# Performance work log

Hardware: AMD Instinct MI355X
Metric: run time of the kernel (lower is better)

## Reference

```python
import jax, jax.numpy as jnp
import numpy as np
import math

F_DIM = 512
N_HEADS = 8
HEAD_DIM = F_DIM // N_HEADS
IMG = 16            # image_size
L = IMG ** 3        # voxel sequence length = 4096
PATCH = 196         # patch_number (ViT 14x14)
VIT_RES = 14
RES = 224           # VIEW_IMAGE_RES
SKETCH_DIM = 768
SIGMA = 1.5         # fixed kernel_size (torch draws randomly when None)
GN_GROUPS = 32


def position_encoding(d_model, length):
    pe = np.zeros((length, d_model), dtype=np.float32)
    position = np.arange(length, dtype=np.float32)[:, None]
    div_term = np.exp(np.arange(0, d_model, 2, dtype=np.float32) * -(math.log(10000.0) / d_model))
    pe[:, 0::2] = np.sin(position * div_term)
    pe[:, 1::2] = np.cos(position * div_term)
    return jnp.asarray(pe)


def get_voxel_coordinates(resolution, size=1.0):
    # centers of a resolution^3 grid spanning [-size/2, size/2]
    idx = np.arange(resolution, dtype=np.float32)
    g = np.stack(np.meshgrid(idx, idx, idx, indexing='ij'), -1).reshape(-1, 3)
    return (g + 0.5) / resolution * size - size / 2.0


VOXEL_PE = position_encoding(F_DIM, L)          # (L, F)
COND_PE = position_encoding(F_DIM, PATCH)       # (S, F)
VOXEL_PTS = jnp.asarray(get_voxel_coordinates(IMG))  # (L, 3)
_vg = np.arange(VIT_RES, dtype=np.float32)
VIT_PIXELS = jnp.asarray(np.stack(np.meshgrid(_vg, _vg, indexing='ij'), -1).reshape(PATCH, 2))  # (S, 2)


def setup_inputs() -> dict:
    key = jax.random.key(0)
    ks = jax.random.split(key, 12)
    B = 8
    s = 0.02
    return {
        'x': jax.random.normal(ks[0], (B, F_DIM, IMG, IMG, IMG), jnp.float32),
        'sketch_feature': jax.random.normal(ks[1], (B, PATCH, SKETCH_DIM), jnp.float32),
        'projection_matrix': jax.random.normal(ks[2], (B, 1, 3, 3), jnp.float32),
        'gn_scale': jnp.ones((F_DIM,), jnp.float32),
        'gn_bias': jnp.zeros((F_DIM,), jnp.float32),
        'conv_w': jax.random.normal(ks[3], (F_DIM, F_DIM, 3, 3, 3), jnp.float32) * s,
        'conv_b': jnp.zeros((F_DIM,), jnp.float32),
        'k_w': jax.random.normal(ks[4], (F_DIM, SKETCH_DIM), jnp.float32) * s,
        'k_b': jnp.zeros((F_DIM,), jnp.float32),
        'v_w': jax.random.normal(ks[5], (F_DIM, SKETCH_DIM), jnp.float32) * s,
        'v_b': jnp.zeros((F_DIM,), jnp.float32),
        'in_proj_w': jax.random.normal(ks[6], (3 * F_DIM, F_DIM), jnp.float32) * s,
        'in_proj_b': jnp.zeros((3 * F_DIM,), jnp.float32),
        'out_w': jax.random.normal(ks[7], (F_DIM, F_DIM), jnp.float32) * s,
        'out_b': jnp.zeros((F_DIM,), jnp.float32),
    }


def _group_norm(x, scale, bias, groups=GN_GROUPS, eps=1e-5):
    B, C = x.shape[0], x.shape[1]
    xr = x.reshape(B, groups, C // groups, -1)
    m = xr.mean(axis=(2, 3), keepdims=True)
    v = xr.var(axis=(2, 3), keepdims=True)
    xn = ((xr - m) / jnp.sqrt(v + eps)).reshape(x.shape)
    shp = (1, C) + (1,) * (x.ndim - 2)
    return xn * scale.reshape(shp) + bias.reshape(shp)


def _attn_mask(projection_matrix):
    # project voxel centers, clamp to pixel grid, threshold cdist to vit patch centers
    P = projection_matrix[:, 0]                                  # (B,3,3)
    pc = jnp.einsum('bij,nj->bni', P, VOXEL_PTS)                 # (B,L,3)
    pixels = pc[..., 0:2] / pc[..., 2:3]
    pixels = jnp.clip(jnp.round(pixels), 0.0, RES - 1.0)         # clamp_pixel
    x_idx = (2.0 * pixels[..., 1:2] + 1.0) / RES * VIT_RES / 2.0
    y_idx = (2.0 * (RES - 1.0 - pixels[..., 0:1]) + 1.0) / RES * VIT_RES / 2.0
    ps = jnp.concatenate([x_idx, y_idx], -1) - 0.5               # (B,L,2)
    dist = jnp.linalg.norm(ps[:, :, None, :] - VIT_PIXELS[None, None], axis=-1)  # (B,L,S)
    return jnp.abs(dist) > (SIGMA - 1e-6)                        # True = masked out


def _forward(x, sketch_feature, projection_matrix, gn_scale, gn_bias, conv_w, conv_b,
             k_w, k_b, v_w, v_b, in_proj_w, in_proj_b, out_w, out_b):
    B = x.shape[0]
    # q path: GroupNorm -> SiLU -> Conv3d(3, pad 1)
    h = jax.nn.silu(_group_norm(x, gn_scale, gn_bias))
    h = jax.lax.conv_general_dilated(h, conv_w, window_strides=(1, 1, 1),
                                     padding=[(1, 1)] * 3,
                                     dimension_numbers=('NCDHW', 'OIDHW', 'NCDHW'))
    h = h + conv_b.reshape(1, F_DIM, 1, 1, 1)
    q = h.reshape(B, F_DIM, L).transpose(0, 2, 1) + VOXEL_PE[None]        # (B,L,F)

    mask = _attn_mask(projection_matrix)                                   # (B,L,S)

    k = sketch_feature @ k_w.T + k_b + COND_PE[None]                       # (B,S,F)
    v = sketch_feature @ v_w.T + v_b + COND_PE[None]

    # nn.MultiheadAttention (eval: no dropout)
    wq, wk, wv = jnp.split(in_proj_w, 3, axis=0)
    bq, bk, bv = jnp.split(in_proj_b, 3, axis=0)
    qh = (q @ wq.T + bq).reshape(B, L, N_HEADS, HEAD_DIM).transpose(0, 2, 1, 3)
    kh = (k @ wk.T + bk).reshape(B, PATCH, N_HEADS, HEAD_DIM).transpose(0, 2, 1, 3)
    vh = (v @ wv.T + bv).reshape(B, PATCH, N_HEADS, HEAD_DIM).transpose(0, 2, 1, 3)

    scores = jnp.einsum('bhld,bhsd->bhls', qh, kh) / math.sqrt(HEAD_DIM)   # (B,H,L,S)
    scores = jnp.where(mask[:, None], -jnp.inf, scores)                    # mask shared over heads
    attn = jax.nn.softmax(scores, axis=-1)
    o = jnp.einsum('bhls,bhsd->bhld', attn, vh)
    o = o.transpose(0, 2, 1, 3).reshape(B, L, F_DIM)
    o = o @ out_w.T + out_b                                                # (B,L,F)
    return o.transpose(0, 2, 1).reshape(B, F_DIM, IMG, IMG, IMG)


def reference(x, sketch_feature, projection_matrix, gn_scale, gn_bias, conv_w, conv_b,
              k_w, k_b, v_w, v_b, in_proj_w, in_proj_b, out_w, out_b):
    return _forward(x, sketch_feature, projection_matrix, gn_scale, gn_bias, conv_w, conv_b,
                    k_w, k_b, v_w, v_b, in_proj_w, in_proj_b, out_w, out_b)
```

## Files before the change

### kernel.cpp

```cpp
#include <hip/hip_runtime.h>

#define DEV static __device__ __forceinline__

typedef unsigned short u16;
typedef unsigned int u32;
typedef unsigned long long u64;
typedef float f32x4 __attribute__((ext_vector_type(4)));
typedef short bfrag __attribute__((ext_vector_type(8)));

#define FD 512
#define LV 4096
#define PV 5832

DEV float b2f(u16 u){ union{ u32 i; float f; } x; x.i = ((u32)u)<<16; return x.f; }
DEV u16 f2b(float f){ union{ float f; u32 i; } x; x.f = f; u32 r = x.i; r += 0x7fffu + ((r>>16)&1u); return (u16)(r>>16); }

DEV void g2l(const void* g, void* s){
  __builtin_amdgcn_global_load_lds((const __attribute__((address_space(1))) void*)g,
                                   (__attribute__((address_space(3))) void*)s, 16, 0, 0);
}

static const size_t o_wt  = 0;
static const size_t o_wq  = 14155776;
static const size_t o_ow  = 14680064;
static const size_t o_vpe = 15204352;
static const size_t o_cpe = 23592960;
static const size_t o_gn  = 23994368;
static const size_t o_mask= 23996416;
static const size_t o_khb = 25044992;
static const size_t o_vhb = 26748928;
static const size_t o_hp  = 36841472;
static const size_t o_qb  = 84617216;
static const size_t o_qh  = 118171648;
static const size_t o_skb = o_qh;
static const size_t o_kwb = o_qh + 2555904;
static const size_t o_vwb = o_qh + 3342336;
static const size_t o_wkb = o_qh + 4128768;
static const size_t o_wvb = o_qh + 4653056;
static const size_t o_ktb = o_qh + 5177344;
static const size_t o_vtb = o_qh + 6881280;

__global__ void pe_kernel(float* __restrict__ pe, int length){
  int l = blockIdx.x;
  int i = threadIdx.x;
  if (l >= length) return;
  const float fac = -0.017988946039015984f;
  float dt = expf((float)(2*i) * fac);
  float ang = (float)l * dt;
  pe[(size_t)l*FD + 2*i]     = sinf(ang);
  pe[(size_t)l*FD + 2*i + 1] = cosf(ang);
}

__global__ void cast_bf16(const float* __restrict__ in, u16* __restrict__ out, int n){
  int i = blockIdx.x*256 + threadIdx.x;
  if (i < n) out[i] = f2b(in[i]);
}

__global__ void convw_prep(const float* __restrict__ cw, u16* __restrict__ wt){
  int idx = blockIdx.x*256 + threadIdx.x;
  const float* src = cw + (size_t)idx*27;
  float v[27];
  #pragma unroll
  for (int k=0;k<27;k++) v[k] = src[k];
  #pragma unroll
  for (int k=0;k<27;k++) wt[(size_t)k*262144 + idx] = f2b(v[k]);
}

__global__ __launch_bounds__(256) void gn_stats(const float* __restrict__ x, float* __restrict__ stats){
  int bg = blockIdx.x;
  const float* base = x + (size_t)bg*65536;
  float s=0.f, q=0.f;
  for (int i=threadIdx.x;i<65536;i+=256){ float v = base[i]; s+=v; q+=v*v; }
  #pragma unroll
  for (int off=32; off>0; off>>=1){ s += __shfl_xor(s,off); q += __shfl_xor(q,off); }
  __shared__ float red[8];
  int w = threadIdx.x>>6;
  if ((threadIdx.x&63)==0){ red[w*2]=s; red[w*2+1]=q; }
  __syncthreads();
  if (threadIdx.x==0){
    float S=red[0]+red[2]+red[4]+red[6];
    float Q=red[1]+red[3]+red[5]+red[7];
    float m = S*(1.f/65536.f);
    float var = Q*(1.f/65536.f) - m*m;
    stats[bg] = m;
    stats[256+bg] = rsqrtf(var + 1e-5f);
  }
}

__global__ __launch_bounds__(256) void gn_apply_b(const float* __restrict__ x,
    const float* __restrict__ stats, const float* __restrict__ sc, const float* __restrict__ bi,
    u16* __restrict__ hp){
  int zb = blockIdx.x, cb = blockIdx.y, b = blockIdx.z;
  const float* xb = x + (size_t)b*FD*LV;
  u16* hpb = hp + (size_t)b*PV*FD;
  int t = threadIdx.x;
  int y = t>>4, xx = t&15;
  size_t hrow = ((size_t)(zb+1)*324 + (size_t)(y+1)*18 + (xx+1))*FD;
  int v = zb*256 + t;
  #pragma unroll 4
  for (int cc=0; cc<64; ++cc){
    int c = cb*64 + cc;
    float val = xb[(size_t)c*LV + v];
    int g = c>>4;
    float m = stats[b*32+g];
    float r = stats[256 + b*32+g];
    float xn = (val - m)*r*sc[c] + bi[c];
    hpb[hrow + c] = f2b(xn / (1.f + expf(-xn)));
  }
}

__global__ __launch_bounds__(256,4) void conv_mfma(const u16* __restrict__ hp,
    const u16* __restrict__ wt, const float* __restrict__ cbias,
    const float* __restrict__ vpe, u16* __restrict__ qb){
  __shared__ __align__(16) u16 Al[8192];
  __shared__ __align__(16) u16 Wl[8192];
  int tid = threadIdx.x;
  int w = tid>>6, l = tid&63;
  int v0 = blockIdx.x*128, n0 = blockIdx.y*128, b = blockIdx.z;
  int swz = ((l&7) ^ ((l>>3)&7))*8;
  size_t abase[4], wbase[4];
  #pragma unroll
  for (int j=0;j<4;j++){
    int r = w*32 + j*8 + (l>>3);
    int v = v0 + r;
    int z = v>>8, yy=(v>>4)&15, xx=v&15;
    abase[j] = ((size_t)b*PV + (size_t)(z*324 + yy*18 + xx))*FD + swz;
    wbase[j] = (size_t)(n0 + r)*FD + swz;
  }
  f32x4 zero4 = {0.f,0.f,0.f,0.f};
  f32x4 acc[4][4];
  #pragma unroll
  for (int i=0;i<4;i++)
    #pragma unroll
    for (int j=0;j<4;j++) acc[i][j] = zero4;
  int wr = (w>>1)*64, wc = (w&1)*64;
  for (int kk=0; kk<216; ++kk){
    int off = kk>>3;
    int ks  = (kk&7)<<6;
    int dz = off/9; int rem = off - dz*9; int dy = rem/3; int dx = rem - dy*3;
    size_t adelta = (size_t)(dz*324 + dy*18 + dx)*FD + ks;
    size_t wdelta = (size_t)off*262144 + ks;
    #pragma unroll
    for (int j=0;j<4;j++){
      g2l(hp + abase[j] + adelta, Al + (w*32 + j*8)*64);
      g2l(wt + wbase[j] + wdelta, Wl + (w*32 + j*8)*64);
    }
    __syncthreads();
    #pragma unroll
    for (int ks2=0; ks2<2; ++ks2){
      bfrag af[4], wf[4];
      #pragma unroll
      for (int i=0;i<4;i++){
        int ra = wr + i*16 + (l&15);
        af[i] = *(const bfrag*)(Al + ra*64 + (((ks2<<2) + (l>>4)) ^ (l&7))*8);
        int rb = wc + i*16 + (l&15);
        wf[i] = *(const bfrag*)(Wl + rb*64 + (((ks2<<2) + (l>>4)) ^ (l&7))*8);
      }
      #pragma unroll
      for (int i=0;i<4;i++)
        #pragma unroll
        for (int j=0;j<4;j++)
          acc[i][j] = __builtin_amdgcn_mfma_f32_16x16x32_bf16(af[i], wf[j], acc[i][j], 0,0,0);
    }
    __syncthreads();
  }
  #pragma unroll
  for (int i=0;i<4;i++)
    #pragma unroll
    for (int j=0;j<4;j++)
      #pragma unroll
      for (int rg=0;rg<4;rg++){
        int row = wr + i*16 + ((l>>4)<<2) + rg;
        int col = wc + j*16 + (l&15);
        int v = v0 + row, n = n0 + col;
        float cv = acc[i][j][rg] + cbias[n] + vpe[(size_t)v*FD + n];
        qb[((size_t)b*LV + v)*FD + n] = f2b(cv);
      }
}

template<bool TRANS>
__global__ __launch_bounds__(256,2) void gemm_mfma(const u16* __restrict__ A, const u16* __restrict__ W,
    const float* __restrict__ bias, void* __restrict__ Cout){
  __shared__ __align__(16) u16 Al[4096];
  __shared__ __align__(16) u16 Wl[4096];
  int tid = threadIdx.x;
  int w = tid>>6, l = tid&63;
  int m0 = blockIdx.x*128, n0 = blockIdx.y*128, b = blockIdx.z;
  int sw_src = (((l&3) ^ ((l>>3)&3)))*8;
  int sw_rd  = (((l>>4) ^ ((l>>1)&3)))*8;
  size_t abase[2], wbase[2];
  #pragma unroll
  for (int j=0;j<2;j++){
    int r = (w*2+j)*16 + (l>>2);
    abase[j] = ((size_t)b*LV + m0 + r)*FD + sw_src;
    wbase[j] = (size_t)(n0 + r)*FD + sw_src;
  }
  f32x4 zero4 = {0.f,0.f,0.f,0.f};
  f32x4 acc[4][4];
  #pragma unroll
  for (int i=0;i<4;i++)
    #pragma unroll
    for (int j=0;j<4;j++) acc[i][j] = zero4;
  int wr = (w>>1)*64, wc = (w&1)*64;
  for (int k0=0; k0<512; k0+=32){
    #pragma unroll
    for (int j=0;j<2;j++){
      g2l(A + abase[j] + k0, Al + (w*2+j)*512);
      g2l(W + wbase[j] + k0, Wl + (w*2+j)*512);
    }
    __syncthreads();
    bfrag af[4], wf[4];
    #pragma unroll
    for (int i=0;i<4;i++){
      int r  = wr + i*16 + (l&15);
      af[i] = *(const bfrag*)(Al + r*32 + sw_rd);
      int cn = wc + i*16 + (l&15);
      wf[i] = *(const bfrag*)(Wl + cn*32 + sw_rd);
    }
    #pragma unroll
    for (int i=0;i<4;i++)
      #pragma unroll
      for (int j=0;j<4;j++)
        acc[i][j] = __builtin_amdgcn_mfma_f32_16x16x32_bf16(af[i], wf[j], acc[i][j], 0,0,0);
    __syncthreads();
  }
  #pragma unroll
  for (int i=0;i<4;i++)
    #pragma unroll
    for (int j=0;j<4;j++)
      #pragma unroll
      for (int rg=0;rg<4;rg++){
        int row = m0 + wr + i*16 + ((l>>4)<<2) + rg;
        int col = n0 + wc + j*16 + (l&15);
        float cv = acc[i][j][rg] + bias[col];
        if constexpr (TRANS)
          ((float*)Cout)[((size_t)b*FD + col)*LV + row] = cv;
        else
          ((u16*)Cout)[((size_t)b*LV + row)*FD + col] = f2b(cv);
      }
}

template<bool OUTF32, bool ADDPE>
__global__ __launch_bounds__(256,2) void gemm_kv(const u16* __restrict__ A, const u16* __restrict__ W,
    const float* __restrict__ bias, const float* __restrict__ pe,
    void* __restrict__ Cout, int K){
  __shared__ __align__(16) u16 Al[4096];
  __shared__ __align__(16) u16 Wl[4096];
  int tid = threadIdx.x;
  int w = tid>>6, l = tid&63;
  int m0 = blockIdx.x*128, n0 = blockIdx.y*128;
  int sw_src = (((l&3) ^ ((l>>3)&3)))*8;
  int sw_rd  = (((l>>4) ^ ((l>>1)&3)))*8;
  size_t abase[2], wbase[2];
  #pragma unroll
  for (int j=0;j<2;j++){
    int r = (w*2+j)*16 + (l>>2);
    abase[j] = (size_t)(m0 + r)*K + sw_src;
    wbase[j] = (size_t)(n0 + r)*K + sw_src;
  }
  f32x4 zero4 = {0.f,0.f,0.f,0.f};
  f32x4 acc[4][4];
  #pragma unroll
  for (int i=0;i<4;i++)
    #pragma unroll
    for (int j=0;j<4;j++) acc[i][j] = zero4;
  int wr = (w>>1)*64, wc = (w&1)*64;
  for (int k0=0; k0<K; k0+=32){
    #pragma unroll
    for (int j=0;j<2;j++){
      g2l(A + abase[j] + k0, Al + (w*2+j)*512);
      g2l(W + wbase[j] + k0, Wl + (w*2+j)*512);
    }
    __syncthreads();
    bfrag af[4], wf[4];
    #pragma unroll
    for (int i=0;i<4;i++){
      int r  = wr + i*16 + (l&15);
      af[i] = *(const bfrag*)(Al + r*32 + sw_rd);
      int cn = wc + i*16 + (l&15);
      wf[i] = *(const bfrag*)(Wl + cn*32 + sw_rd);
    }
    #pragma unroll
    for (int i=0;i<4;i++)
      #pragma unroll
      for (int j=0;j<4;j++)
        acc[i][j] = __builtin_amdgcn_mfma_f32_16x16x32_bf16(af[i], wf[j], acc[i][j], 0,0,0);
    __syncthreads();
  }
  #pragma unroll
  for (int i=0;i<4;i++)
    #pragma unroll
    for (int j=0;j<4;j++)
      #pragma unroll
      for (int rg=0;rg<4;rg++){
        int row = m0 + wr + i*16 + ((l>>4)<<2) + rg;
        int col = n0 + wc + j*16 + (l&15);
        float cv = acc[i][j][rg] + bias[col];
        if constexpr (ADDPE) cv += pe[(size_t)(row % 196)*FD + col];
        if constexpr (OUTF32) ((float*)Cout)[(size_t)row*FD + col] = cv;
        else                  ((u16*)Cout)[(size_t)row*FD + col] = f2b(cv);
      }
}

__global__ __launch_bounds__(256) void mask_kernel(const float* __restrict__ proj, u64* __restrict__ maskb){
  int idx = blockIdx.x*256 + threadIdx.x;
  int b = idx >> 12, v = idx & 4095;
  float P[9];
  #pragma unroll
  for (int j=0;j<9;j++) P[j] = proj[b*9 + j];
  int zi=v>>8, yi=(v>>4)&15, xi=v&15;
  float pt0 = ((float)zi + 0.5f)/16.0f - 0.5f;
  float pt1 = ((float)yi + 0.5f)/16.0f - 0.5f;
  float pt2 = ((float)xi + 0.5f)/16.0f - 0.5f;
  float pc0 = __fadd_rn(__fadd_rn(__fmul_rn(P[0],pt0), __fmul_rn(P[1],pt1)), __fmul_rn(P[2],pt2));
  float pc1 = __fadd_rn(__fadd_rn(__fmul_rn(P[3],pt0), __fmul_rn(P[4],pt1)), __fmul_rn(P[5],pt2));
  float pc2 = __fadd_rn(__fadd_rn(__fmul_rn(P[6],pt0), __fmul_rn(P[7],pt1)), __fmul_rn(P[8],pt2));
  float r0 = __fdiv_rn(pc0, pc2);
  float r1 = __fdiv_rn(pc1, pc2);
  float px0 = fminf(fmaxf(rintf(r0), 0.f), 223.f);
  float px1 = fminf(fmaxf(rintf(r1), 0.f), 223.f);
  float x_idx = __fmul_rn(__fdiv_rn(__fadd_rn(__fmul_rn(2.f,px1),1.f), 224.f), 14.f) * 0.5f;
  float y_idx = __fmul_rn(__fdiv_rn(__fadd_rn(__fmul_rn(2.f,__fadd_rn(223.f,-px0)),1.f), 224.f), 14.f) * 0.5f;
  float ps0 = __fadd_rn(x_idx, -0.5f);
  float ps1 = __fadd_rn(y_idx, -0.5f);
  const float TH = 1.4999990463256836f;
  u64 abits[4] = {0,0,0,0};
  #pragma unroll 1
  for (int s=0;s<196;s++){
    int si = s/14, sj = s - si*14;
    float d0 = __fadd_rn(ps0, -(float)si);
    float d1 = __fadd_rn(ps1, -(float)sj);
    float dist = sqrtf(__fadd_rn(__fmul_rn(d0,d0), __fmul_rn(d1,d1)));
    if (!(fabsf(dist) > TH)) abits[s>>6] |= (1ull << (s&63));
  }
  u64* out = maskb + (size_t)idx*4;
  out[0]=abits[0]; out[1]=abits[1]; out[2]=abits[2]; out[3]=abits[3];
}

__global__ __launch_bounds__(256) void attn_lit(const u16* __restrict__ qh,
    const u16* __restrict__ khb, const u16* __restrict__ vhb,
    const u64* __restrict__ maskb, u16* __restrict__ obuf){
  int v = blockIdx.x*256 + threadIdx.x;
  int h = blockIdx.y, b = blockIdx.z;
  const u64* mrow = maskb + ((size_t)b*LV + v)*4;
  u64 abits[4] = {mrow[0], mrow[1], mrow[2], mrow[3]};

  float qr[64];
  {
    const uint4* qp = (const uint4*)(qh + ((size_t)b*LV + v)*FD + h*64);
    #pragma unroll
    for (int c=0;c<8;c++){
      uint4 u = qp[c];
      qr[c*8+0]=b2f((u16)(u.x&0xffffu)); qr[c*8+1]=b2f((u16)(u.x>>16));
      qr[c*8+2]=b2f((u16)(u.y&0xffffu)); qr[c*8+3]=b2f((u16)(u.y>>16));
      qr[c*8+4]=b2f((u16)(u.z&0xffffu)); qr[c*8+5]=b2f((u16)(u.z>>16));
      qr[c*8+6]=b2f((u16)(u.w&0xffffu)); qr[c*8+7]=b2f((u16)(u.w>>16));
    }
  }
  const u16* kb = khb + (size_t)(b*196)*FD + h*64;
  const u16* vb = vhb + (size_t)(b*196)*FD + h*64;
  float o[64];
  #pragma unroll
  for (int d=0;d<64;d++) o[d]=0.f;
  float ssum = 0.f;
  for (int s=0;s<196;s++){
    if (!((abits[s>>6] >> (s&63)) & 1ull)) continue;
    const uint4* kr = (const uint4*)(kb + (size_t)s*FD);
    float dot = 0.f;
    #pragma unroll
    for (int c=0;c<8;c++){
      uint4 u = kr[c];
      dot += qr[c*8+0]*b2f((u16)(u.x&0xffffu)) + qr[c*8+1]*b2f((u16)(u.x>>16))
           + qr[c*8+2]*b2f((u16)(u.y&0xffffu)) + qr[c*8+3]*b2f((u16)(u.y>>16))
           + qr[c*8+4]*b2f((u16)(u.z&0xffffu)) + qr[c*8+5]*b2f((u16)(u.z>>16))
           + qr[c*8+6]*b2f((u16)(u.w&0xffffu)) + qr[c*8+7]*b2f((u16)(u.w>>16));
    }
    float e = expf(dot*0.125f);
    ssum += e;
    const uint4* vr = (const uint4*)(vb + (size_t)s*FD);
    #pragma unroll
    for (int c=0;c<8;c++){
      uint4 u = vr[c];
      o[c*8+0] += e*b2f((u16)(u.x&0xffffu)); o[c*8+1] += e*b2f((u16)(u.x>>16));
      o[c*8+2] += e*b2f((u16)(u.y&0xffffu)); o[c*8+3] += e*b2f((u16)(u.y>>16));
      o[c*8+4] += e*b2f((u16)(u.z&0xffffu)); o[c*8+5] += e*b2f((u16)(u.z>>16));
      o[c*8+6] += e*b2f((u16)(u.w&0xffffu)); o[c*8+7] += e*b2f((u16)(u.w>>16));
    }
  }
  float inv = (ssum > 0.f) ? 1.f/ssum : 0.f;
  u32* op = (u32*)(obuf + ((size_t)b*LV + v)*FD + h*64);
  #pragma unroll
  for (int c=0;c<32;c++){
    u32 lo = f2b(o[c*2]*inv);
    u32 hi = f2b(o[c*2+1]*inv);
    op[c] = lo | (hi<<16);
  }
}

extern "C" void kernel_launch(void* const* d_in, const int* in_sizes, int n_in,
                              void* d_out, int out_size, void* d_ws, size_t ws_size,
                              hipStream_t stream) {
  (void)in_sizes; (void)n_in; (void)out_size; (void)ws_size;
  const float* x_in  = (const float*)d_in[0];
  const float* sketch= (const float*)d_in[1];
  const float* projm = (const float*)d_in[2];
  const float* gnsc  = (const float*)d_in[3];
  const float* gnbi  = (const float*)d_in[4];
  const float* convw = (const float*)d_in[5];
  const float* convb = (const float*)d_in[6];
  const float* kw_in = (const float*)d_in[7];
  const float* kb_in = (const float*)d_in[8];
  const float* vw_in = (const float*)d_in[9];
  const float* vb_in = (const float*)d_in[10];
  const float* ipw   = (const float*)d_in[11];
  const float* ipb   = (const float*)d_in[12];
  const float* ow_in = (const float*)d_in[13];
  const float* ob_in = (const float*)d_in[14];
  char* ws = (char*)d_ws;
  u16*   wt   = (u16*)(ws + o_wt);
  u16*   Wq   = (u16*)(ws + o_wq);
  u16*   Ow   = (u16*)(ws + o_ow);
  float* vpe  = (float*)(ws + o_vpe);
  float* cpe  = (float*)(ws + o_cpe);
  float* stats= (float*)(ws + o_gn);
  u64*   maskb= (u64*)(ws + o_mask);
  u16*   khb  = (u16*)(ws + o_khb);
  u16*   vhb  = (u16*)(ws + o_vhb);
  u16*   hp   = (u16*)(ws + o_hp);
  u16*   qb   = (u16*)(ws + o_qb);
  u16*   qhb  = (u16*)(ws + o_qh);
  u16*   Skb  = (u16*)(ws + o_skb);
  u16*   Kwb  = (u16*)(ws + o_kwb);
  u16*   Vwb  = (u16*)(ws + o_vwb);
  u16*   Wkb  = (u16*)(ws + o_wkb);
  u16*   Wvb  = (u16*)(ws + o_wvb);
  u16*   ktb  = (u16*)(ws + o_ktb);
  u16*   vtb  = (u16*)(ws + o_vtb);
  u16*   obuf = qb;

  hipMemsetAsync(hp, 0, 47775744, stream);
  hipMemsetAsync((char*)Skb + 2408448, 0, 147456, stream);
  convw_prep<<<1024,256,0,stream>>>(convw, wt);
  cast_bf16<<<1024,256,0,stream>>>(ipw,          Wq,  262144);
  cast_bf16<<<1024,256,0,stream>>>(ow_in,        Ow,  262144);
  cast_bf16<<<4704,256,0,stream>>>(sketch,       Skb, 1204224);
  cast_bf16<<<1536,256,0,stream>>>(kw_in,        Kwb, 393216);
  cast_bf16<<<1536,256,0,stream>>>(vw_in,        Vwb, 393216);
  cast_bf16<<<1024,256,0,stream>>>(ipw + 262144, Wkb, 262144);
  cast_bf16<<<1024,256,0,stream>>>(ipw + 524288, Wvb, 262144);
  pe_kernel<<<4096,256,0,stream>>>(vpe, 4096);
  pe_kernel<<<196,256,0,stream>>>(cpe, 196);
  gn_stats<<<256,256,0,stream>>>(x_in, stats);
  mask_kernel<<<128,256,0,stream>>>(projm, maskb);
  gemm_kv<false,true ><<<dim3(13,4),256,0,stream>>>(Skb, Kwb, kb_in,      cpe,     ktb, 768);
  gemm_kv<false,true ><<<dim3(13,4),256,0,stream>>>(Skb, Vwb, vb_in,      cpe,     vtb, 768);
  gemm_kv<false,false><<<dim3(13,4),256,0,stream>>>(ktb, Wkb, ipb + 512,  nullptr, khb, 512);
  gemm_kv<false,false><<<dim3(13,4),256,0,stream>>>(vtb, Wvb, ipb + 1024, nullptr, vhb, 512);

  gn_apply_b<<<dim3(16,8,8),256,0,stream>>>(x_in, stats, gnsc, gnbi, hp);
  conv_mfma<<<dim3(32,4,8),256,0,stream>>>(hp, wt, convb, vpe, qb);
  gemm_mfma<false><<<dim3(32,4,8),256,0,stream>>>(qb, Wq, ipb, qhb);
  attn_lit<<<dim3(16,8,8),256,0,stream>>>(qhb, khb, vhb, maskb, obuf);
  gemm_mfma<true ><<<dim3(32,4,8),256,0,stream>>>(obuf, Ow, ob_in, d_out);
}
```

Baseline: 804.2 us.

## Merge prep kernels and batch K/V GEMMs to cut launch count

Folds the eight cast kernels and the conv-weight transpose into one prep_all launch, merges the positional-encoding and mask kernels into geom_prep, and runs the K and V projection GEMMs as one launch each using blockIdx.z to pick the operand set. This removes many small launches and their serialization gaps, and lets the tiny K/V GEMMs fill more CUs. The transposed output GEMM now writes float4 vectors instead of scalar stores. The merged kernels use block-range dispatch, which adds some branching and hardcoded block boundaries.

```diff
diff --git a/kernel.cpp b/kernel.cpp
--- a/kernel.cpp
+++ b/kernel.cpp
@@ -40,270 +40,43 @@
 static const size_t o_ktb = o_qh + 5177344;
 static const size_t o_vtb = o_qh + 6881280;
 
-__global__ void pe_kernel(float* __restrict__ pe, int length){
-  int l = blockIdx.x;
-  int i = threadIdx.x;
-  if (l >= length) return;
-  const float fac = -0.017988946039015984f;
-  float dt = expf((float)(2*i) * fac);
-  float ang = (float)l * dt;
-  pe[(size_t)l*FD + 2*i]     = sinf(ang);
-  pe[(size_t)l*FD + 2*i + 1] = cosf(ang);
-}
-
-__global__ void cast_bf16(const float* __restrict__ in, u16* __restrict__ out, int n){
-  int i = blockIdx.x*256 + threadIdx.x;
-  if (i < n) out[i] = f2b(in[i]);
-}
-
-__global__ void convw_prep(const float* __restrict__ cw, u16* __restrict__ wt){
-  int idx = blockIdx.x*256 + threadIdx.x;
-  const float* src = cw + (size_t)idx*27;
-  float v[27];
-  #pragma unroll
-  for (int k=0;k<27;k++) v[k] = src[k];
-  #pragma unroll
-  for (int k=0;k<27;k++) wt[(size_t)k*262144 + idx] = f2b(v[k]);
-}
-
-__global__ __launch_bounds__(256) void gn_stats(const float* __restrict__ x, float* __restrict__ stats){
-  int bg = blockIdx.x;
-  const float* base = x + (size_t)bg*65536;
-  float s=0.f, q=0.f;
-  for (int i=threadIdx.x;i<65536;i+=256){ float v = base[i]; s+=v; q+=v*v; }
-  #pragma unroll
-  for (int off=32; off>0; off>>=1){ s += __shfl_xor(s,off); q += __shfl_xor(q,off); }
-  __shared__ float red[8];
-  int w = threadIdx.x>>6;
-  if ((threadIdx.x&63)==0){ red[w*2]=s; red[w*2+1]=q; }
-  __syncthreads();
-  if (threadIdx.x==0){
-    float S=red[0]+red[2]+red[4]+red[6];
-    float Q=red[1]+red[3]+red[5]+red[7];
-    float m = S*(1.f/65536.f);
-    float var = Q*(1.f/65536.f) - m*m;
-    stats[bg] = m;
-    stats[256+bg] = rsqrtf(var + 1e-5f);
-  }
-}
-
-__global__ __launch_bounds__(256) void gn_apply_b(const float* __restrict__ x,
-    const float* __restrict__ stats, const float* __restrict__ sc, const float* __restrict__ bi,
-    u16* __restrict__ hp){
-  int zb = blockIdx.x, cb = blockIdx.y, b = blockIdx.z;
-  const float* xb = x + (size_t)b*FD*LV;
-  u16* hpb = hp + (size_t)b*PV*FD;
-  int t = threadIdx.x;
-  int y = t>>4, xx = t&15;
-  size_t hrow = ((size_t)(zb+1)*324 + (size_t)(y+1)*18 + (xx+1))*FD;
-  int v = zb*256 + t;
-  #pragma unroll 4
-  for (int cc=0; cc<64; ++cc){
-    int c = cb*64 + cc;
-    float val = xb[(size_t)c*LV + v];
-    int g = c>>4;
-    float m = stats[b*32+g];
-    float r = stats[256 + b*32+g];
-    float xn = (val - m)*r*sc[c] + bi[c];
-    hpb[hrow + c] = f2b(xn / (1.f + expf(-xn)));
-  }
-}
-
-__global__ __launch_bounds__(256,4) void conv_mfma(const u16* __restrict__ hp,
-    const u16* __restrict__ wt, const float* __restrict__ cbias,
-    const float* __restrict__ vpe, u16* __restrict__ qb){
-  __shared__ __align__(16) u16 Al[8192];
-  __shared__ __align__(16) u16 Wl[8192];
-  int tid = threadIdx.x;
-  int w = tid>>6, l = tid&63;
-  int v0 = blockIdx.x*128, n0 = blockIdx.y*128, b = blockIdx.z;
-  int swz = ((l&7) ^ ((l>>3)&7))*8;
-  size_t abase[4], wbase[4];
-  #pragma unroll
-  for (int j=0;j<4;j++){
-    int r = w*32 + j*8 + (l>>3);
-    int v = v0 + r;
-    int z = v>>8, yy=(v>>4)&15, xx=v&15;
-    abase[j] = ((size_t)b*PV + (size_t)(z*324 + yy*18 + xx))*FD + swz;
-    wbase[j] = (size_t)(n0 + r)*FD + swz;
-  }
-  f32x4 zero4 = {0.f,0.f,0.f,0.f};
-  f32x4 acc[4][4];
-  #pragma unroll
-  for (int i=0;i<4;i++)
-    #pragma unroll
-    for (int j=0;j<4;j++) acc[i][j] = zero4;
-  int wr = (w>>1)*64, wc = (w&1)*64;
-  for (int kk=0; kk<216; ++kk){
-    int off = kk>>3;
-    int ks  = (kk&7)<<6;
-    int dz = off/9; int rem = off - dz*9; int dy = rem/3; int dx = rem - dy*3;
-    size_t adelta = (size_t)(dz*324 + dy*18 + dx)*FD + ks;
-    size_t wdelta = (size_t)off*262144 + ks;
-    #pragma unroll
-    for (int j=0;j<4;j++){
-      g2l(hp + abase[j] + adelta, Al + (w*32 + j*8)*64);
-      g2l(wt + wbase[j] + wdelta, Wl + (w*32 + j*8)*64);
-    }
-    __syncthreads();
-    #pragma unroll
-    for (int ks2=0; ks2<2; ++ks2){
-      bfrag af[4], wf[4];
-      #pragma unroll
-      for (int i=0;i<4;i++){
-        int ra = wr + i*16 + (l&15);
-        af[i] = *(const bfrag*)(Al + ra*64 + (((ks2<<2) + (l>>4)) ^ (l&7))*8);
-        int rb = wc + i*16 + (l&15);
-        wf[i] = *(const bfrag*)(Wl + rb*64 + (((ks2<<2) + (l>>4)) ^ (l&7))*8);
-      }
-      #pragma unroll
-      for (int i=0;i<4;i++)
-        #pragma unroll
-        for (int j=0;j<4;j++)
-          acc[i][j] = __builtin_amdgcn_mfma_f32_16x16x32_bf16(af[i], wf[j], acc[i][j], 0,0,0);
-    }
-    __syncthreads();
-  }
-  #pragma unroll
-  for (int i=0;i<4;i++)
-    #pragma unroll
-    for (int j=0;j<4;j++)
-      #pragma unroll
-      for (int rg=0;rg<4;rg++){
-        int row = wr + i*16 + ((l>>4)<<2) + rg;
-        int col = wc + j*16 + (l&15);
-        int v = v0 + row, n = n0 + col;
-        float cv = acc[i][j][rg] + cbias[n] + vpe[(size_t)v*FD + n];
-        qb[((size_t)b*LV + v)*FD + n] = f2b(cv);
-      }
-}
-
-template<bool TRANS>
-__global__ __launch_bounds__(256,2) void gemm_mfma(const u16* __restrict__ A, const u16* __restrict__ W,
-    const float* __restrict__ bias, void* __restrict__ Cout){
-  __shared__ __align__(16) u16 Al[4096];
-  __shared__ __align__(16) u16 Wl[4096];
-  int tid = threadIdx.x;
-  int w = tid>>6, l = tid&63;
-  int m0 = blockIdx.x*128, n0 = blockIdx.y*128, b = blockIdx.z;
-  int sw_src = (((l&3) ^ ((l>>3)&3)))*8;
-  int sw_rd  = (((l>>4) ^ ((l>>1)&3)))*8;
-  size_t abase[2], wbase[2];
-  #pragma unroll
-  for (int j=0;j<2;j++){
-    int r = (w*2+j)*16 + (l>>2);
-    abase[j] = ((size_t)b*LV + m0 + r)*FD + sw_src;
-    wbase[j] = (size_t)(n0 + r)*FD + sw_src;
-  }
-  f32x4 zero4 = {0.f,0.f,0.f,0.f};
-  f32x4 acc[4][4];
-  #pragma unroll
-  for (int i=0;i<4;i++)
-    #pragma unroll
-    for (int j=0;j<4;j++) acc[i][j] = zero4;
-  int wr = (w>>1)*64, wc = (w&1)*64;
-  for (int k0=0; k0<512; k0+=32){
-    #pragma unroll
-    for (int j=0;j<2;j++){
-      g2l(A + abase[j] + k0, Al + (w*2+j)*512);
-      g2l(W + wbase[j] + k0, Wl + (w*2+j)*512);
-    }
-    __syncthreads();
-    bfrag af[4], wf[4];
-    #pragma unroll
-    for (int i=0;i<4;i++){
-      int r  = wr + i*16 + (l&15);
-      af[i] = *(const bfrag*)(Al + r*32 + sw_rd);
-      int cn = wc + i*16 + (l&15);
-      wf[i] = *(const bfrag*)(Wl + cn*32 + sw_rd);
-    }
-    #pragma unroll
-    for (int i=0;i<4;i++)
-      #pragma unroll
-      for (int j=0;j<4;j++)
-        acc[i][j] = __builtin_amdgcn_mfma_f32_16x16x32_bf16(af[i], wf[j], acc[i][j], 0,0,0);
-    __syncthreads();
-  }
-  #pragma unroll
-  for (int i=0;i<4;i++)
-    #pragma unroll
-    for (int j=0;j<4;j++)
-      #pragma unroll
-      for (int rg=0;rg<4;rg++){
-        int row = m0 + wr + i*16 + ((l>>4)<<2) + rg;
-        int col = n0 + wc + j*16 + (l&15);
-        float cv = acc[i][j][rg] + bias[col];
-        if constexpr (TRANS)
-          ((float*)Cout)[((size_t)b*FD + col)*LV + row] = cv;
-        else
-          ((u16*)Cout)[((size_t)b*LV + row)*FD + col] = f2b(cv);
-      }
-}
-
-template<bool OUTF32, bool ADDPE>
-__global__ __launch_bounds__(256,2) void gemm_kv(const u16* __restrict__ A, const u16* __restrict__ W,
-    const float* __restrict__ bias, const float* __restrict__ pe,
-    void* __restrict__ Cout, int K){
-  __shared__ __align__(16) u16 Al[4096];
-  __shared__ __align__(16) u16 Wl[4096];
-  int tid = threadIdx.x;
-  int w = tid>>6, l = tid&63;
-  int m0 = blockIdx.x*128, n0 = blockIdx.y*128;
-  int sw_src = (((l&3) ^ ((l>>3)&3)))*8;
-  int sw_rd  = (((l>>4) ^ ((l>>1)&3)))*8;
-  size_t abase[2], wbase[2];
-  #pragma unroll
-  for (int j=0;j<2;j++){
-    int r = (w*2+j)*16 + (l>>2);
-    abase[j] = (size_t)(m0 + r)*K + sw_src;
-    wbase[j] = (size_t)(n0 + r)*K + sw_src;
-  }
-  f32x4 zero4 = {0.f,0.f,0.f,0.f};
-  f32x4 acc[4][4];
-  #pragma unroll
-  for (int i=0;i<4;i++)
-    #pragma unroll
-    for (int j=0;j<4;j++) acc[i][j] = zero4;
-  int wr = (w>>1)*64, wc = (w&1)*64;
-  for (int k0=0; k0<K; k0+=32){
-    #pragma unroll
-    for (int j=0;j<2;j++){
-      g2l(A + abase[j] + k0, Al + (w*2+j)*512);
-      g2l(W + wbase[j] + k0, Wl + (w*2+j)*512);
-    }
-    __syncthreads();
-    bfrag af[4], wf[4];
-    #pragma unroll
-    for (int i=0;i<4;i++){
-      int r  = wr + i*16 + (l&15);
-      af[i] = *(const bfrag*)(Al + r*32 + sw_rd);
-      int cn = wc + i*16 + (l&15);
-      wf[i] = *(const bfrag*)(Wl + cn*32 + sw_rd);
-    }
-    #pragma unroll
-    for (int i=0;i<4;i++)
-      #pragma unroll
-      for (int j=0;j<4;j++)
-        acc[i][j] = __builtin_amdgcn_mfma_f32_16x16x32_bf16(af[i], wf[j], acc[i][j], 0,0,0);
-    __syncthreads();
-  }
-  #pragma unroll
-  for (int i=0;i<4;i++)
-    #pragma unroll
-    for (int j=0;j<4;j++)
-      #pragma unroll
-      for (int rg=0;rg<4;rg++){
-        int row = m0 + wr + i*16 + ((l>>4)<<2) + rg;
-        int col = n0 + wc + j*16 + (l&15);
-        float cv = acc[i][j][rg] + bias[col];
-        if constexpr (ADDPE) cv += pe[(size_t)(row % 196)*FD + col];
-        if constexpr (OUTF32) ((float*)Cout)[(size_t)row*FD + col] = cv;
-        else                  ((u16*)Cout)[(size_t)row*FD + col] = f2b(cv);
-      }
-}
-
-__global__ __launch_bounds__(256) void mask_kernel(const float* __restrict__ proj, u64* __restrict__ maskb){
-  int idx = blockIdx.x*256 + threadIdx.x;
+__global__ __launch_bounds__(256) void prep_all(const float* __restrict__ convw,
+    const float* __restrict__ ipw, const float* __restrict__ ow,
+    const float* __restrict__ sketch, const float* __restrict__ kw, const float* __restrict__ vw,
+    u16* __restrict__ wt, u16* __restrict__ Wq, u16* __restrict__ Ow, u16* __restrict__ Skb,
+    u16* __restrict__ Kwb, u16* __restrict__ Vwb, u16* __restrict__ Wkb, u16* __restrict__ Wvb){
+  int blk = blockIdx.x, t = threadIdx.x;
+  if (blk < 1024){
+    int idx = blk*256 + t;
+    const float* src = convw + (size_t)idx*27;
+    float v[27];
+    #pragma unroll
+    for (int k=0;k<27;k++) v[k] = src[k];
+    #pragma unroll
+    for (int k=0;k<27;k++) wt[(size_t)k*262144 + idx] = f2b(v[k]);
+  } else if (blk < 2048){ int i=(blk-1024)*256+t;  Wq[i]  = f2b(ipw[i]); }
+  else if (blk < 3072){   int i=(blk-2048)*256+t;  Ow[i]  = f2b(ow[i]); }
+  else if (blk < 7776){   int i=(blk-3072)*256+t;  if (i<1204224) Skb[i] = f2b(sketch[i]); }
+  else if (blk < 9312){   int i=(blk-7776)*256+t;  Kwb[i] = f2b(kw[i]); }
+  else if (blk < 10848){  int i=(blk-9312)*256+t;  Vwb[i] = f2b(vw[i]); }
+  else if (blk < 11872){  int i=(blk-10848)*256+t; Wkb[i] = f2b(ipw[262144+i]); }
+  else {                  int i=(blk-11872)*256+t; Wvb[i] = f2b(ipw[524288+i]); }
+}
+
+__global__ __launch_bounds__(256) void geom_prep(float* __restrict__ vpe, float* __restrict__ cpe,
+    const float* __restrict__ proj, u64* __restrict__ maskb){
+  int blk = blockIdx.x, t = threadIdx.x;
+  if (blk < 4292){
+    float* pe = (blk < 4096) ? vpe : cpe;
+    int l = (blk < 4096) ? blk : blk - 4096;
+    const float fac = -0.017988946039015984f;
+    float dt = expf((float)(2*t) * fac);
+    float ang = (float)l * dt;
+    pe[(size_t)l*FD + 2*t]     = sinf(ang);
+    pe[(size_t)l*FD + 2*t + 1] = cosf(ang);
+    return;
+  }
+  int idx = (blk-4292)*256 + t;
   int b = idx >> 12, v = idx & 4095;
   float P[9];
   #pragma unroll
@@ -335,6 +108,251 @@
   }
   u64* out = maskb + (size_t)idx*4;
   out[0]=abits[0]; out[1]=abits[1]; out[2]=abits[2]; out[3]=abits[3];
+}
+
+__global__ __launch_bounds__(256) void gn_stats(const float* __restrict__ x, float* __restrict__ stats){
+  int bg = blockIdx.x;
+  const float* base = x + (size_t)bg*65536;
+  float s=0.f, q=0.f;
+  for (int i=threadIdx.x;i<65536;i+=256){ float v = base[i]; s+=v; q+=v*v; }
+  #pragma unroll
+  for (int off=32; off>0; off>>=1){ s += __shfl_xor(s,off); q += __shfl_xor(q,off); }
+  __shared__ float red[8];
+  int w = threadIdx.x>>6;
+  if ((threadIdx.x&63)==0){ red[w*2]=s; red[w*2+1]=q; }
+  __syncthreads();
+  if (threadIdx.x==0){
+    float S=red[0]+red[2]+red[4]+red[6];
+    float Q=red[1]+red[3]+red[5]+red[7];
+    float m = S*(1.f/65536.f);
+    float var = Q*(1.f/65536.f) - m*m;
+    stats[bg] = m;
+    stats[256+bg] = rsqrtf(var + 1e-5f);
+  }
+}
+
+__global__ __launch_bounds__(256) void gn_apply_b(const float* __restrict__ x,
+    const float* __restrict__ stats, const float* __restrict__ sc, const float* __restrict__ bi,
+    u16* __restrict__ hp){
+  int zb = blockIdx.x, cb = blockIdx.y, b = blockIdx.z;
+  const float* xb = x + (size_t)b*FD*LV;
+  u16* hpb = hp + (size_t)b*PV*FD;
+  int t = threadIdx.x;
+  int y = t>>4, xx = t&15;
+  size_t hrow = ((size_t)(zb+1)*324 + (size_t)(y+1)*18 + (xx+1))*FD;
+  int v = zb*256 + t;
+  #pragma unroll 4
+  for (int cc=0; cc<64; ++cc){
+    int c = cb*64 + cc;
+    float val = xb[(size_t)c*LV + v];
+    int g = c>>4;
+    float m = stats[b*32+g];
+    float r = stats[256 + b*32+g];
+    float xn = (val - m)*r*sc[c] + bi[c];
+    hpb[hrow + c] = f2b(xn / (1.f + expf(-xn)));
+  }
+}
+
+__global__ __launch_bounds__(256,4) void conv_mfma(const u16* __restrict__ hp,
+    const u16* __restrict__ wt, const float* __restrict__ cbias,
+    const float* __restrict__ vpe, u16* __restrict__ qb){
+  __shared__ __align__(16) u16 Al[8192];
+  __shared__ __align__(16) u16 Wl[8192];
+  int tid = threadIdx.x;
+  int w = tid>>6, l = tid&63;
+  int v0 = blockIdx.x*128, n0 = blockIdx.y*128, b = blockIdx.z;
+  int swz = ((l&7) ^ ((l>>3)&7))*8;
+  size_t abase[4], wbase[4];
+  #pragma unroll
+  for (int j=0;j<4;j++){
+    int r = w*32 + j*8 + (l>>3);
+    int v = v0 + r;
+    int z = v>>8, yy=(v>>4)&15, xx=v&15;
+    abase[j] = ((size_t)b*PV + (size_t)(z*324 + yy*18 + xx))*FD + swz;
+    wbase[j] = (size_t)(n0 + r)*FD + swz;
+  }
+  f32x4 zero4 = {0.f,0.f,0.f,0.f};
+  f32x4 acc[4][4];
+  #pragma unroll
+  for (int i=0;i<4;i++)
+    #pragma unroll
+    for (int j=0;j<4;j++) acc[i][j] = zero4;
+  int wr = (w>>1)*64, wc = (w&1)*64;
+  for (int kk=0; kk<216; ++kk){
+    int off = kk>>3;
+    int ks  = (kk&7)<<6;
+    int dz = off/9; int rem = off - dz*9; int dy = rem/3; int dx = rem - dy*3;
+    size_t adelta = (size_t)(dz*324 + dy*18 + dx)*FD + ks;
+    size_t wdelta = (size_t)off*262144 + ks;
+    #pragma unroll
+    for (int j=0;j<4;j++){
+      g2l(hp + abase[j] + adelta, Al + (w*32 + j*8)*64);
+      g2l(wt + wbase[j] + wdelta, Wl + (w*32 + j*8)*64);
+    }
+    __syncthreads();
+    #pragma unroll
+    for (int ks2=0; ks2<2; ++ks2){
+      bfrag af[4], wf[4];
+      #pragma unroll
+      for (int i=0;i<4;i++){
+        int ra = wr + i*16 + (l&15);
+        af[i] = *(const bfrag*)(Al + ra*64 + (((ks2<<2) + (l>>4)) ^ (l&7))*8);
+        int rb = wc + i*16 + (l&15);
+        wf[i] = *(const bfrag*)(Wl + rb*64 + (((ks2<<2) + (l>>4)) ^ (l&7))*8);
+      }
+      #pragma unroll
+      for (int i=0;i<4;i++)
+        #pragma unroll
+        for (int j=0;j<4;j++)
+          acc[i][j] = __builtin_amdgcn_mfma_f32_16x16x32_bf16(af[i], wf[j], acc[i][j], 0,0,0);
+    }
+    __syncthreads();
+  }
+  #pragma unroll
+  for (int i=0;i<4;i++)
+    #pragma unroll
+    for (int j=0;j<4;j++)
+      #pragma unroll
+      for (int rg=0;rg<4;rg++){
+        int row = wr + i*16 + ((l>>4)<<2) + rg;
+        int col = wc + j*16 + (l&15);
+        int v = v0 + row, n = n0 + col;
+        float cv = acc[i][j][rg] + cbias[n] + vpe[(size_t)v*FD + n];
+        qb[((size_t)b*LV + v)*FD + n] = f2b(cv);
+      }
+}
+
+template<bool TRANS>
+__global__ __launch_bounds__(256,2) void gemm_mfma(const u16* __restrict__ A, const u16* __restrict__ W,
+    const float* __restrict__ bias, void* __restrict__ Cout){
+  __shared__ __align__(16) u16 Al[4096];
+  __shared__ __align__(16) u16 Wl[4096];
+  int tid = threadIdx.x;
+  int w = tid>>6, l = tid&63;
+  int m0 = blockIdx.x*128, n0 = blockIdx.y*128, b = blockIdx.z;
+  int sw_src = (((l&3) ^ ((l>>3)&3)))*8;
+  int sw_rd  = (((l>>4) ^ ((l>>1)&3)))*8;
+  size_t abase[2], wbase[2];
+  #pragma unroll
+  for (int j=0;j<2;j++){
+    int r = (w*2+j)*16 + (l>>2);
+    abase[j] = ((size_t)b*LV + m0 + r)*FD + sw_src;
+    wbase[j] = (size_t)(n0 + r)*FD + sw_src;
+  }
+  f32x4 zero4 = {0.f,0.f,0.f,0.f};
+  f32x4 acc[4][4];
+  #pragma unroll
+  for (int i=0;i<4;i++)
+    #pragma unroll
+    for (int j=0;j<4;j++) acc[i][j] = zero4;
+  int wr = (w>>1)*64, wc = (w&1)*64;
+  for (int k0=0; k0<512; k0+=32){
+    #pragma unroll
+    for (int j=0;j<2;j++){
+      g2l(A + abase[j] + k0, Al + (w*2+j)*512);
+      g2l(W + wbase[j] + k0, Wl + (w*2+j)*512);
+    }
+    __syncthreads();
+    bfrag af[4], wf[4];
+    #pragma unroll
+    for (int i=0;i<4;i++){
+      int r  = wr + i*16 + (l&15);
+      af[i] = *(const bfrag*)(Al + r*32 + sw_rd);
+      int cn = wc + i*16 + (l&15);
+      wf[i] = *(const bfrag*)(Wl + cn*32 + sw_rd);
+    }
+    #pragma unroll
+    for (int i=0;i<4;i++)
+      #pragma unroll
+      for (int j=0;j<4;j++)
+        acc[i][j] = __builtin_amdgcn_mfma_f32_16x16x32_bf16(af[i], wf[j], acc[i][j], 0,0,0);
+    __syncthreads();
+  }
+  #pragma unroll
+  for (int i=0;i<4;i++)
+    #pragma unroll
+    for (int j=0;j<4;j++){
+      if constexpr (TRANS){
+        int row = m0 + wr + i*16 + ((l>>4)<<2);
+        int col = n0 + wc + j*16 + (l&15);
+        float bv = bias[col];
+        float4 val = { acc[i][j][0]+bv, acc[i][j][1]+bv, acc[i][j][2]+bv, acc[i][j][3]+bv };
+        *(float4*)&(((float*)Cout)[((size_t)b*FD + col)*LV + row]) = val;
+      } else {
+        #pragma unroll
+        for (int rg=0;rg<4;rg++){
+          int row = m0 + wr + i*16 + ((l>>4)<<2) + rg;
+          int col = n0 + wc + j*16 + (l&15);
+          ((u16*)Cout)[((size_t)b*LV + row)*FD + col] = f2b(acc[i][j][rg] + bias[col]);
+        }
+      }
+    }
+}
+
+template<bool ADDPE>
+__global__ __launch_bounds__(256,2) void gemm_kv(const u16* __restrict__ A0, const u16* __restrict__ A1,
+    const u16* __restrict__ W0, const u16* __restrict__ W1,
+    const float* __restrict__ b0, const float* __restrict__ b1,
+    const float* __restrict__ pe, u16* __restrict__ C0, u16* __restrict__ C1, int K){
+  const u16* A = blockIdx.z ? A1 : A0;
+  const u16* W = blockIdx.z ? W1 : W0;
+  const float* bias = blockIdx.z ? b1 : b0;
+  u16* Cout = blockIdx.z ? C1 : C0;
+  __shared__ __align__(16) u16 Al[4096];
+  __shared__ __align__(16) u16 Wl[4096];
+  int tid = threadIdx.x;
+  int w = tid>>6, l = tid&63;
+  int m0 = blockIdx.x*128, n0 = blockIdx.y*128;
+  int sw_src = (((l&3) ^ ((l>>3)&3)))*8;
+  int sw_rd  = (((l>>4) ^ ((l>>1)&3)))*8;
+  size_t abase[2], wbase[2];
+  #pragma unroll
+  for (int j=0;j<2;j++){
+    int r = (w*2+j)*16 + (l>>2);
+    abase[j] = (size_t)(m0 + r)*K + sw_src;
+    wbase[j] = (size_t)(n0 + r)*K + sw_src;
+  }
+  f32x4 zero4 = {0.f,0.f,0.f,0.f};
+  f32x4 acc[4][4];
+  #pragma unroll
+  for (int i=0;i<4;i++)
+    #pragma unroll
+    for (int j=0;j<4;j++) acc[i][j] = zero4;
+  int wr = (w>>1)*64, wc = (w&1)*64;
+  for (int k0=0; k0<K; k0+=32){
+    #pragma unroll
+    for (int j=0;j<2;j++){
+      g2l(A + abase[j] + k0, Al + (w*2+j)*512);
+      g2l(W + wbase[j] + k0, Wl + (w*2+j)*512);
+    }
+    __syncthreads();
+    bfrag af[4], wf[4];
+    #pragma unroll
+    for (int i=0;i<4;i++){
+      int r  = wr + i*16 + (l&15);
+      af[i] = *(const bfrag*)(Al + r*32 + sw_rd);
+      int cn = wc + i*16 + (l&15);
+      wf[i] = *(const bfrag*)(Wl + cn*32 + sw_rd);
+    }
+    #pragma unroll
+    for (int i=0;i<4;i++)
+      #pragma unroll
+      for (int j=0;j<4;j++)
+        acc[i][j] = __builtin_amdgcn_mfma_f32_16x16x32_bf16(af[i], wf[j], acc[i][j], 0,0,0);
+    __syncthreads();
+  }
+  #pragma unroll
+  for (int i=0;i<4;i++)
+    #pragma unroll
+    for (int j=0;j<4;j++)
+      #pragma unroll
+      for (int rg=0;rg<4;rg++){
+        int row = m0 + wr + i*16 + ((l>>4)<<2) + rg;
+        int col = n0 + wc + j*16 + (l&15);
+        float cv = acc[i][j][rg] + bias[col];
+        if constexpr (ADDPE) cv += pe[(size_t)(row % 196)*FD + col];
+        Cout[(size_t)row*FD + col] = f2b(cv);
+      }
 }
 
 __global__ __launch_bounds__(256) void attn_lit(const u16* __restrict__ qh,
@@ -440,22 +458,12 @@
 
   hipMemsetAsync(hp, 0, 47775744, stream);
   hipMemsetAsync((char*)Skb + 2408448, 0, 147456, stream);
-  convw_prep<<<1024,256,0,stream>>>(convw, wt);
-  cast_bf16<<<1024,256,0,stream>>>(ipw,          Wq,  262144);
-  cast_bf16<<<1024,256,0,stream>>>(ow_in,        Ow,  262144);
-  cast_bf16<<<4704,256,0,stream>>>(sketch,       Skb, 1204224);
-  cast_bf16<<<1536,256,0,stream>>>(kw_in,        Kwb, 393216);
-  cast_bf16<<<1536,256,0,stream>>>(vw_in,        Vwb, 393216);
-  cast_bf16<<<1024,256,0,stream>>>(ipw + 262144, Wkb, 262144);
-  cast_bf16<<<1024,256,0,stream>>>(ipw + 524288, Wvb, 262144);
-  pe_kernel<<<4096,256,0,stream>>>(vpe, 4096);
-  pe_kernel<<<196,256,0,stream>>>(cpe, 196);
+  prep_all<<<12896,256,0,stream>>>(convw, ipw, ow_in, sketch, kw_in, vw_in,
+                                   wt, Wq, Ow, Skb, Kwb, Vwb, Wkb, Wvb);
+  geom_prep<<<4420,256,0,stream>>>(vpe, cpe, projm, maskb);
   gn_stats<<<256,256,0,stream>>>(x_in, stats);
-  mask_kernel<<<128,256,0,stream>>>(projm, maskb);
-  gemm_kv<false,true ><<<dim3(13,4),256,0,stream>>>(Skb, Kwb, kb_in,      cpe,     ktb, 768);
-  gemm_kv<false,true ><<<dim3(13,4),256,0,stream>>>(Skb, Vwb, vb_in,      cpe,     vtb, 768);
-  gemm_kv<false,false><<<dim3(13,4),256,0,stream>>>(ktb, Wkb, ipb + 512,  nullptr, khb, 512);
-  gemm_kv<false,false><<<dim3(13,4),256,0,stream>>>(vtb, Wvb, ipb + 1024, nullptr, vhb, 512);
+  gemm_kv<true ><<<dim3(13,4,2),256,0,stream>>>(Skb, Skb, Kwb, Vwb, kb_in, vb_in, cpe, ktb, vtb, 768);
+  gemm_kv<false><<<dim3(13,4,2),256,0,stream>>>(ktb, vtb, Wkb, Wvb, ipb+512, ipb+1024, nullptr, khb, vhb, 512);
 
   gn_apply_b<<<dim3(16,8,8),256,0,stream>>>(x_in, stats, gnsc, gnbi, hp);
   conv_mfma<<<dim3(32,4,8),256,0,stream>>>(hp, wt, convb, vpe, qb);
```

New measurement: 775.0 us. 1.04x faster.
